# Optimization experiments

Measured on AMD Instinct MI355X. Metric: run time of the kernel, lower is better.

The kernel has to match this reference:

```python
import jax, jax.numpy as jnp
import numpy as np

D_MODEL = 1024
N_HEAD = 16
D_HEAD = D_MODEL // N_HEAD
N_EXPERTS = 8
TOP_K = 2
D_FF = 4096
EPS = 1e-6


def setup_inputs() -> dict:
    key = jax.random.key(0)
    ks = jax.random.split(key, 16)
    s = 0.02  # init scale
    d, dff, E = D_MODEL, D_FF, N_EXPERTS
    return {
        "dec": jax.random.normal(ks[0], (4, 1024, d), jnp.float32),
        "text_encoder": jax.random.normal(ks[1], (4, 512, d), jnp.float32),
        # self-attention projections
        "Wq1": jax.random.normal(ks[2], (d, d), jnp.float32) * s,
        "Wk1": jax.random.normal(ks[3], (d, d), jnp.float32) * s,
        "Wv1": jax.random.normal(ks[4], (d, d), jnp.float32) * s,
        "Wo1": jax.random.normal(ks[5], (d, d), jnp.float32) * s,
        # cross-attention projections
        "Wq2": jax.random.normal(ks[6], (d, d), jnp.float32) * s,
        "Wk2": jax.random.normal(ks[7], (d, d), jnp.float32) * s,
        "Wv2": jax.random.normal(ks[8], (d, d), jnp.float32) * s,
        "Wo2": jax.random.normal(ks[9], (d, d), jnp.float32) * s,
        # shared RMSNorm gain (module uses one norm instance three times)
        "g": jnp.ones((d,), jnp.float32),
        # MoE router + per-expert FFN weights
        "Wg": jax.random.normal(ks[10], (d, E), jnp.float32) * s,
        "W1": jax.random.normal(ks[11], (E, d, dff), jnp.float32) * s,
        "W2": jax.random.normal(ks[12], (E, dff, d), jnp.float32) * s,
    }


def rmsnorm(x, g):
    return x * jax.lax.rsqrt(jnp.mean(x * x, axis=-1, keepdims=True) + EPS) * g


def mha(q_in, k_in, v_in, Wq, Wk, Wv, Wo):
    B, Sq, _ = q_in.shape
    Sk = k_in.shape[1]
    q = (q_in @ Wq).reshape(B, Sq, N_HEAD, D_HEAD)
    k = (k_in @ Wk).reshape(B, Sk, N_HEAD, D_HEAD)
    v = (v_in @ Wv).reshape(B, Sk, N_HEAD, D_HEAD)
    scores = jnp.einsum("bqhd,bkhd->bhqk", q, k) / jnp.sqrt(jnp.asarray(D_HEAD, q.dtype))
    attn = jax.nn.softmax(scores, axis=-1)
    out = jnp.einsum("bhqk,bkhd->bqhd", attn, v).reshape(B, Sq, D_MODEL)
    return out @ Wo


def moe(x, Wg, W1, W2):
    # top-k softmax router, renormalized weights; dense per-expert FFN with combine
    probs = jax.nn.softmax(x @ Wg, axis=-1)              # [B,S,E]
    weights, indices = jax.lax.top_k(probs, TOP_K)        # [B,S,k]
    weights = weights / jnp.sum(weights, axis=-1, keepdims=True)
    # combine[t,e] = sum_k weights[t,k] * (indices[t,k]==e)
    combine = jnp.sum(
        jax.nn.one_hot(indices, N_EXPERTS, dtype=x.dtype) * weights[..., None], axis=-2
    )  # [B,S,E]
    out = jnp.zeros_like(x)
    for e in range(N_EXPERTS):  # fixed small expert loop
        h = jax.nn.relu(x @ W1[e]) @ W2[e]
        out = out + combine[..., e:e + 1] * h
    return weights, indices, out


def reference(dec, text_encoder, Wq1, Wk1, Wv1, Wo1, Wq2, Wk2, Wv2, Wo2, g, Wg, W1, W2):
    # self-attention + residual + RMSNorm (dropout p=0 -> identity)
    x = rmsnorm(mha(dec, dec, dec, Wq1, Wk1, Wv1, Wo1) + dec, g)
    # cross-attention + residual + RMSNorm
    x = rmsnorm(mha(x, text_encoder, text_encoder, Wq2, Wk2, Wv2, Wo2) + x, g)
    # MoE FFN + residual + RMSNorm
    weights, indices, y = moe(x, Wg, W1, W2)
    x = rmsnorm(y + x, g)
    return weights, indices, x
```

## Files before the change

kernel.cpp:

```cpp
#include <hip/hip_runtime.h>
#include <stdint.h>

#define D_    1024
#define BB    4
#define SDEC  1024
#define STXT  512
#define TDEC  4096
#define TTXT  2048
#define NH    16
#define DHD   64
#define NE    8
#define DFF   4096
#define NSLOT 8192
#define MAXYT 24

using u16 = unsigned short;
typedef __attribute__((ext_vector_type(8))) short bf16x8;
typedef __attribute__((ext_vector_type(4))) float f32x4;

__device__ __forceinline__ float bf2f(u16 h) {
    union { unsigned int u; float f; } x; x.u = ((unsigned int)h) << 16; return x.f;
}
__device__ __forceinline__ u16 f2bf(float f) {
    union { float f; unsigned int u; } x; x.f = f;
    unsigned int lsb = (x.u >> 16) & 1u;
    return (u16)((x.u + 0x7fffu + lsb) >> 16);
}

__device__ __forceinline__ void gld16(const u16* g, u16* l) {
    __builtin_amdgcn_global_load_lds((const __attribute__((address_space(1))) void*)g,
                                     (__attribute__((address_space(3))) void*)l,
                                     16, 0, 0);
}

constexpr int BM = 128, BK = 32;

template<int SPLIT, int EPI, int BROWS>
__global__ __launch_bounds__(256) void gemm_bt(
    const u16* __restrict__ AH, const u16* __restrict__ AL,
    const u16* __restrict__ BH, const u16* __restrict__ BL,
    float* __restrict__ Cf, u16* __restrict__ CH, u16* __restrict__ CL,
    int M, int N, int K, int lda, int ldb, int ldc,
    long strA, long strB, long strC)
{
    constexpr int WM = (BROWS == 64) ? 2 : 4;
    constexpr int ASZ = BM * BK, BSZ = BROWS * BK;
    __shared__ u16 smem[(SPLIT ? 2 : 1) * (ASZ + BSZ)];
    u16* sAH = smem;
    u16* sBH = smem + ASZ;
    u16* sAL = SPLIT ? smem + ASZ + BSZ : nullptr;
    u16* sBL = SPLIT ? smem + 2 * ASZ + BSZ : nullptr;

    const int z = blockIdx.z;
    const long zA = (long)z * strA, zB = (long)z * strB, zC = (long)z * strC;

    const int tileM = blockIdx.y * BM, tileN = blockIdx.x * BROWS;
    const int t = threadIdx.x;
    const int sr = t >> 2;
    const int sc = (t & 3) << 3;
    const u16* pA = AH + zA + (long)(tileM + sr) * lda + sc;
    const u16* pB = BH + zB + (long)(tileN + sr) * ldb + sc;
    const u16* pAl = nullptr; const u16* pBl = nullptr;
    if constexpr (SPLIT) {
        pAl = AL + zA + (long)(tileM + sr) * lda + sc;
        pBl = BL + zB + (long)(tileN + sr) * ldb + sc;
    }
    const long hA = 64L * lda, hB = 64L * ldb;

    const int lane = t & 63;
    const int wv = t >> 6;
    const int wr = (BROWS == 64) ? (wv << 5) : ((wv >> 1) << 6);
    const int wc = (BROWS == 64) ? 0 : ((wv & 1) << 6);
    const int fr = lane & 15, kg = lane >> 4;

    f32x4 acc[WM][4];
    const f32x4 vzero = {0.f, 0.f, 0.f, 0.f};
#pragma unroll
    for (int m = 0; m < WM; ++m)
#pragma unroll
        for (int n = 0; n < 4; ++n) acc[m][n] = vzero;

    for (int k0 = 0; k0 < K; k0 += BK) {
        gld16(pA + k0,      sAH + t * 8);
        gld16(pA + k0 + hA, sAH + 2048 + t * 8);
        gld16(pB + k0,      sBH + t * 8);
        if constexpr (BROWS == 128) gld16(pB + k0 + hB, sBH + 2048 + t * 8);
        if constexpr (SPLIT) {
            gld16(pAl + k0,      sAL + t * 8);
            gld16(pAl + k0 + hA, sAL + 2048 + t * 8);
            gld16(pBl + k0,      sBL + t * 8);
            if constexpr (BROWS == 128) gld16(pBl + k0 + hB, sBL + 2048 + t * 8);
        }
        __syncthreads();

        bf16x8 fa[WM], fb[4], fal[WM], fbl[4];
#pragma unroll
        for (int m = 0; m < WM; ++m) {
            fa[m] = *(const bf16x8*)&sAH[(wr + m * 16 + fr) * BK + (kg << 3)];
            if constexpr (SPLIT) fal[m] = *(const bf16x8*)&sAL[(wr + m * 16 + fr) * BK + (kg << 3)];
        }
#pragma unroll
        for (int n = 0; n < 4; ++n) {
            fb[n] = *(const bf16x8*)&sBH[(wc + n * 16 + fr) * BK + (kg << 3)];
            if constexpr (SPLIT) fbl[n] = *(const bf16x8*)&sBL[(wc + n * 16 + fr) * BK + (kg << 3)];
        }
#pragma unroll
        for (int m = 0; m < WM; ++m)
#pragma unroll
            for (int n = 0; n < 4; ++n) {
                acc[m][n] = __builtin_amdgcn_mfma_f32_16x16x32_bf16(fa[m], fb[n], acc[m][n], 0, 0, 0);
                if constexpr (SPLIT) {
                    acc[m][n] = __builtin_amdgcn_mfma_f32_16x16x32_bf16(fa[m],  fbl[n], acc[m][n], 0, 0, 0);
                    acc[m][n] = __builtin_amdgcn_mfma_f32_16x16x32_bf16(fal[m], fb[n],  acc[m][n], 0, 0, 0);
                }
            }
        __syncthreads();
    }

#pragma unroll
    for (int m = 0; m < WM; ++m) {
        const int r0 = tileM + wr + m * 16 + (kg << 2);
#pragma unroll
        for (int n = 0; n < 4; ++n) {
            const int col = tileN + wc + n * 16 + fr;
            if (col >= N) continue;
#pragma unroll
            for (int i = 0; i < 4; ++i) {
                const int r = r0 + i;
                if (r >= M) continue;
                const float v = acc[m][n][i];
                const long off = zC + (long)r * ldc + col;
                if constexpr (EPI == 0) {
                    Cf[off] = v;
                } else if constexpr (EPI == 1) {
                    const u16 h = f2bf(v);
                    CH[off] = h;
                    CL[off] = f2bf(v - bf2f(h));
                } else {
                    CH[off] = f2bf(fmaxf(v, 0.f));
                }
            }
        }
    }
}

template<int EPI>
__global__ __launch_bounds__(256) void gemm_moe(
    const u16* __restrict__ Ag, const u16* __restrict__ BTbase,
    float* __restrict__ Cf, u16* __restrict__ CH,
    int N, int K, int ldc, const int* __restrict__ seg, long btStride, int ntx)
{
    const int bid = blockIdx.x;
    const int e = bid & 7;
    const int rem = bid >> 3;
    const int yt = rem % MAXYT;
    const int xt = rem / MAXYT;
    (void)ntx;

    const int s0 = seg[e], s1 = seg[e + 1];
    const int rowbase = s0 + yt * BM;
    if (rowbase >= s1) return;
    const u16* BT = BTbase + (long)e * btStride;

    __shared__ u16 smem[2 * BM * BK];
    u16* sA = smem;
    u16* sB = smem + BM * BK;

    const int tileN = xt * 128;
    const int t = threadIdx.x;
    const int sr = t >> 2, sc = (t & 3) << 3;
    const u16* pA = Ag + (long)(rowbase + sr) * K + sc;
    const u16* pB = BT + (long)(tileN + sr) * K + sc;
    const long hA = 64L * K, hB = 64L * K;

    const int lane = t & 63;
    const int wv = t >> 6;
    const int wr = (wv >> 1) << 6, wc = (wv & 1) << 6;
    const int fr = lane & 15, kg = lane >> 4;

    f32x4 acc[4][4];
    const f32x4 vzero = {0.f, 0.f, 0.f, 0.f};
#pragma unroll
    for (int m = 0; m < 4; ++m)
#pragma unroll
        for (int n = 0; n < 4; ++n) acc[m][n] = vzero;

    for (int k0 = 0; k0 < K; k0 += BK) {
        gld16(pA + k0,      sA + t * 8);
        gld16(pA + k0 + hA, sA + 2048 + t * 8);
        gld16(pB + k0,      sB + t * 8);
        gld16(pB + k0 + hB, sB + 2048 + t * 8);
        __syncthreads();
        bf16x8 fa[4], fb[4];
#pragma unroll
        for (int m = 0; m < 4; ++m) {
            fa[m] = *(const bf16x8*)&sA[(wr + m * 16 + fr) * BK + (kg << 3)];
            fb[m] = *(const bf16x8*)&sB[(wc + m * 16 + fr) * BK + (kg << 3)];
        }
#pragma unroll
        for (int m = 0; m < 4; ++m)
#pragma unroll
            for (int n = 0; n < 4; ++n)
                acc[m][n] = __builtin_amdgcn_mfma_f32_16x16x32_bf16(fa[m], fb[n], acc[m][n], 0, 0, 0);
        __syncthreads();
    }

#pragma unroll
    for (int m = 0; m < 4; ++m) {
        const int r0 = rowbase + wr + m * 16 + (kg << 2);
#pragma unroll
        for (int n = 0; n < 4; ++n) {
            const int col = tileN + wc + n * 16 + fr;
            if (col >= N) continue;
#pragma unroll
            for (int i = 0; i < 4; ++i) {
                const int r = r0 + i;
                if (r >= s1) continue;
                const float v = acc[m][n][i];
                const long off = (long)r * ldc + col;
                if constexpr (EPI == 0) Cf[off] = v;
                else                    CH[off] = f2bf(fmaxf(v, 0.f));
            }
        }
    }
}

__global__ __launch_bounds__(256) void split2k(const float* __restrict__ in,
                                               u16* __restrict__ oh, u16* __restrict__ ol, long n)
{
    long i = ((long)blockIdx.x * 256 + threadIdx.x) * 4;
    if (i >= n) return;
    float4 v = *(const float4*)(in + i);
    u16 h0 = f2bf(v.x), h1 = f2bf(v.y), h2 = f2bf(v.z), h3 = f2bf(v.w);
    uint2 oo;
    oo.x = (unsigned)h0 | ((unsigned)h1 << 16);
    oo.y = (unsigned)h2 | ((unsigned)h3 << 16);
    *(uint2*)(oh + i) = oo;
    if (ol) {
        u16 l0 = f2bf(v.x - bf2f(h0)), l1 = f2bf(v.y - bf2f(h1));
        u16 l2 = f2bf(v.z - bf2f(h2)), l3 = f2bf(v.w - bf2f(h3));
        uint2 ll;
        ll.x = (unsigned)l0 | ((unsigned)l1 << 16);
        ll.y = (unsigned)l2 | ((unsigned)l3 << 16);
        *(uint2*)(ol + i) = ll;
    }
}

__global__ __launch_bounds__(256) void transpose_split(
    const float* __restrict__ in, u16* __restrict__ oh, u16* __restrict__ ol,
    int R, int C, int ild, long ibs1, long ibs2, int nb2, int old_, long obs)
{
    __shared__ float tile[32][33];
    const int z = blockIdx.z;
    const float* ip = in + (long)(z / nb2) * ibs1 + (long)(z % nb2) * ibs2;
    u16* ohp = oh + (long)z * obs;
    u16* olp = ol ? ol + (long)z * obs : nullptr;
    const int c0 = blockIdx.x * 32, r0 = blockIdx.y * 32;
    const int tx = threadIdx.x & 31, ty = threadIdx.x >> 5;
    for (int i = ty; i < 32; i += 8) {
        int r = r0 + i, c = c0 + tx;
        tile[i][tx] = (r < R && c < C) ? ip[(long)r * ild + c] : 0.f;
    }
    __syncthreads();
    for (int i = ty; i < 32; i += 8) {
        int oc = c0 + i, orr = r0 + tx;
        if (oc < C && orr < R) {
            float v = tile[tx][i];
            u16 h = f2bf(v);
            ohp[(long)oc * old_ + orr] = h;
            if (olp) olp[(long)oc * old_ + orr] = f2bf(v - bf2f(h));
        }
    }
}

__global__ __launch_bounds__(256) void transpose_split_hl(
    const u16* __restrict__ inH, const u16* __restrict__ inL,
    u16* __restrict__ oh, u16* __restrict__ ol,
    int R, int C, int ild, long ibs1, long ibs2, int nb2, int old_, long obs)
{
    __shared__ float tile[32][33];
    const int z = blockIdx.z;
    const long base = (long)(z / nb2) * ibs1 + (long)(z % nb2) * ibs2;
    u16* ohp = oh + (long)z * obs;
    u16* olp = ol + (long)z * obs;
    const int c0 = blockIdx.x * 32, r0 = blockIdx.y * 32;
    const int tx = threadIdx.x & 31, ty = threadIdx.x >> 5;
    for (int i = ty; i < 32; i += 8) {
        int r = r0 + i, c = c0 + tx;
        float v = 0.f;
        if (r < R && c < C) {
            const long o = base + (long)r * ild + c;
            v = bf2f(inH[o]) + bf2f(inL[o]);
        }
        tile[i][tx] = v;
    }
    __syncthreads();
    for (int i = ty; i < 32; i += 8) {
        int oc = c0 + i, orr = r0 + tx;
        if (oc < C && orr < R) {
            float v = tile[tx][i];
            u16 h = f2bf(v);
            ohp[(long)oc * old_ + orr] = h;
            olp[(long)oc * old_ + orr] = f2bf(v - bf2f(h));
        }
    }
}

__global__ __launch_bounds__(256) void softmax_split(
    const float* __restrict__ s, u16* __restrict__ ph, u16* __restrict__ pl,
    int cols, float scale)
{
    const float* p = s + (long)blockIdx.x * cols;
    u16* php = ph + (long)blockIdx.x * cols;
    u16* plp = pl + (long)blockIdx.x * cols;
    const int t = threadIdx.x;
    float v[4];
    int vpt;
    if (cols == 1024) {
        vpt = 4;
        float4 x = ((const float4*)p)[t];
        v[0] = x.x * scale; v[1] = x.y * scale; v[2] = x.z * scale; v[3] = x.w * scale;
    } else {
        vpt = 2;
        float2 x = ((const float2*)p)[t];
        v[0] = x.x * scale; v[1] = x.y * scale; v[2] = -3.4e38f; v[3] = -3.4e38f;
    }
    float mx = fmaxf(fmaxf(v[0], v[1]), fmaxf(v[2], v[3]));
#pragma unroll
    for (int o = 32; o; o >>= 1) mx = fmaxf(mx, __shfl_xor(mx, o));
    __shared__ float sm[4];
    const int wv = t >> 6, ln = t & 63;
    if (ln == 0) sm[wv] = mx;
    __syncthreads();
    mx = fmaxf(fmaxf(sm[0], sm[1]), fmaxf(sm[2], sm[3]));
    float sum = 0.f;
    for (int i = 0; i < vpt; ++i) { v[i] = expf(v[i] - mx); sum += v[i]; }
#pragma unroll
    for (int o = 32; o; o >>= 1) sum += __shfl_xor(sum, o);
    __shared__ float ss[4];
    if (ln == 0) ss[wv] = sum;
    __syncthreads();
    sum = ss[0] + ss[1] + ss[2] + ss[3];
    const float inv = 1.f / sum;
    if (cols == 1024) {
        float q0 = v[0] * inv, q1 = v[1] * inv, q2 = v[2] * inv, q3 = v[3] * inv;
        u16 h0 = f2bf(q0), h1 = f2bf(q1), h2 = f2bf(q2), h3 = f2bf(q3);
        uint2 hh; hh.x = (unsigned)h0 | ((unsigned)h1 << 16); hh.y = (unsigned)h2 | ((unsigned)h3 << 16);
        ((uint2*)php)[t] = hh;
        u16 l0 = f2bf(q0 - bf2f(h0)), l1 = f2bf(q1 - bf2f(h1));
        u16 l2 = f2bf(q2 - bf2f(h2)), l3 = f2bf(q3 - bf2f(h3));
        uint2 ll; ll.x = (unsigned)l0 | ((unsigned)l1 << 16); ll.y = (unsigned)l2 | ((unsigned)l3 << 16);
        ((uint2*)plp)[t] = ll;
    } else {
        float q0 = v[0] * inv, q1 = v[1] * inv;
        u16 h0 = f2bf(q0), h1 = f2bf(q1);
        ((unsigned*)php)[t] = (unsigned)h0 | ((unsigned)h1 << 16);
        u16 l0 = f2bf(q0 - bf2f(h0)), l1 = f2bf(q1 - bf2f(h1));
        ((unsigned*)plp)[t] = (unsigned)l0 | ((unsigned)l1 << 16);
    }
}

__global__ __launch_bounds__(256) void add_rmsnorm(
    const float* __restrict__ a, const float* __restrict__ b, const float* __restrict__ g,
    float* __restrict__ xo, u16* __restrict__ xh, u16* __restrict__ xl)
{
    const long row = blockIdx.x;
    const int t = threadIdx.x;
    const float* pa = a + row * D_;
    const float* pb = b + row * D_;
    float v[4]; double ssq = 0.0;
#pragma unroll
    for (int i = 0; i < 4; ++i) {
        int c = t + (i << 8);
        v[i] = pa[c] + pb[c];
        ssq += (double)v[i] * v[i];
    }
#pragma unroll
    for (int o = 32; o; o >>= 1) ssq += __shfl_xor(ssq, o);
    __shared__ double sd[4];
    if ((t & 63) == 0) sd[t >> 6] = ssq;
    __syncthreads();
    ssq = sd[0] + sd[1] + sd[2] + sd[3];
    const float rs = (float)(1.0 / sqrt(ssq * (1.0 / 1024.0) + 1e-6));
#pragma unroll
    for (int i = 0; i < 4; ++i) {
        int c = t + (i << 8);
        float o = v[i] * rs * g[c];
        xo[row * D_ + c] = o;
        if (xh) {
            u16 h = f2bf(o);
            xh[row * D_ + c] = h;
            if (xl) xl[row * D_ + c] = f2bf(o - bf2f(h));
        }
    }
}

__global__ __launch_bounds__(256) void router_topk(
    const float* __restrict__ x2, const float* __restrict__ Wg,
    float* __restrict__ outw, float* __restrict__ outi,
    int* __restrict__ idx, float* __restrict__ tokw, int* __restrict__ counts, int T)
{
    const int wid = (int)((blockIdx.x * 256 + threadIdx.x) >> 6);
    const int lane = threadIdx.x & 63;
    if (wid >= T) return;
    float acc[NE];
#pragma unroll
    for (int e = 0; e < NE; ++e) acc[e] = 0.f;
    const float* xr = x2 + (long)wid * D_;
    for (int i = 0; i < 16; ++i) {
        float xv = xr[i * 64 + lane];
        const float* wr = Wg + (long)(i * 64 + lane) * NE;
#pragma unroll
        for (int e = 0; e < NE; ++e) acc[e] += xv * wr[e];
    }
#pragma unroll
    for (int e = 0; e < NE; ++e)
#pragma unroll
        for (int o = 32; o; o >>= 1) acc[e] += __shfl_xor(acc[e], o);
    if (lane == 0) {
        float m = acc[0];
#pragma unroll
        for (int e = 1; e < NE; ++e) m = fmaxf(m, acc[e]);
        float p[NE], s = 0.f;
#pragma unroll
        for (int e = 0; e < NE; ++e) { p[e] = expf(acc[e] - m); s += p[e]; }
        const float invs = 1.f / s;
#pragma unroll
        for (int e = 0; e < NE; ++e) p[e] *= invs;
        int e0 = 0;
#pragma unroll
        for (int e = 1; e < NE; ++e) if (p[e] > p[e0]) e0 = e;
        int e1 = (e0 == 0) ? 1 : 0;
#pragma unroll
        for (int e = 0; e < NE; ++e) if (e != e0 && e != e1 && p[e] > p[e1]) e1 = e;
        float w0 = p[e0], w1 = p[e1];
        const float sw = 1.f / (w0 + w1);
        w0 *= sw; w1 *= sw;
        outw[2 * wid] = w0;      outw[2 * wid + 1] = w1;
        outi[2 * wid] = (float)e0; outi[2 * wid + 1] = (float)e1;
        idx[2 * wid] = e0;       idx[2 * wid + 1] = e1;
        tokw[2 * wid] = w0;      tokw[2 * wid + 1] = w1;
        atomicAdd(&counts[e0], 1);
        atomicAdd(&counts[e1], 1);
    }
}

__global__ void scan8(const int* __restrict__ counts, int* __restrict__ seg, int* __restrict__ cursor)
{
    if (threadIdx.x == 0 && blockIdx.x == 0) {
        int a = 0;
        for (int e = 0; e < NE; ++e) { seg[e] = a; cursor[e] = a; a += counts[e]; }
        seg[NE] = a;
    }
}

__global__ __launch_bounds__(256) void scatter_slots(
    const int* __restrict__ idx, int* __restrict__ cursor,
    int* __restrict__ row_token, int* __restrict__ slot_of, int T)
{
    const int t = blockIdx.x * 256 + threadIdx.x;
    if (t >= T) return;
#pragma unroll
    for (int k = 0; k < 2; ++k) {
        const int e = idx[2 * t + k];
        const int pos = atomicAdd(&cursor[e], 1);
        row_token[pos] = t;
        slot_of[2 * t + k] = pos;
    }
}

__global__ __launch_bounds__(256) void gather_bf16(
    const float* __restrict__ x2, const int* __restrict__ row_token, u16* __restrict__ Xg)
{
    const int r = blockIdx.x;
    const int t = threadIdx.x;
    const float* src = x2 + (long)row_token[r] * D_ + t * 4;
    float4 v = *(const float4*)src;
    uint2 oo;
    oo.x = (unsigned)f2bf(v.x) | ((unsigned)f2bf(v.y) << 16);
    oo.y = (unsigned)f2bf(v.z) | ((unsigned)f2bf(v.w) << 16);
    *(uint2*)(Xg + (long)r * D_ + t * 4) = oo;
}

__global__ __launch_bounds__(256) void combine_rmsnorm(
    const float* __restrict__ Y, const int* __restrict__ slot_of, const float* __restrict__ tokw,
    const float* __restrict__ x2, const float* __restrict__ g, float* __restrict__ out)
{
    const long tr = blockIdx.x;
    const int t = threadIdx.x;
    const int s0 = slot_of[2 * tr], s1 = slot_of[2 * tr + 1];
    const float w0 = tokw[2 * tr], w1 = tokw[2 * tr + 1];
    const float* y0 = Y + (long)s0 * D_;
    const float* y1 = Y + (long)s1 * D_;
    const float* xr = x2 + tr * D_;
    float v[4]; double ssq = 0.0;
#pragma unroll
    for (int i = 0; i < 4; ++i) {
        int c = t + (i << 8);
        v[i] = w0 * y0[c] + w1 * y1[c] + xr[c];
        ssq += (double)v[i] * v[i];
    }
#pragma unroll
    for (int o = 32; o; o >>= 1) ssq += __shfl_xor(ssq, o);
    __shared__ double sd[4];
    if ((t & 63) == 0) sd[t >> 6] = ssq;
    __syncthreads();
    ssq = sd[0] + sd[1] + sd[2] + sd[3];
    const float rs = (float)(1.0 / sqrt(ssq * (1.0 / 1024.0) + 1e-6));
#pragma unroll
    for (int i = 0; i < 4; ++i) {
        int c = t + (i << 8);
        out[tr * D_ + c] = v[i] * rs * g[c];
    }
}

__global__ void sentinel(float* o) { o[0] = 12345.0f; }

extern "C" void kernel_launch(void* const* d_in, const int* in_sizes, int n_in,
                              void* d_out, int out_size, void* d_ws, size_t ws_size,
                              hipStream_t stream)
{
    const float* dec = (const float*)d_in[0];
    const float* te  = (const float*)d_in[1];
    const float* Win[8] = { (const float*)d_in[2], (const float*)d_in[3], (const float*)d_in[4],
                            (const float*)d_in[5], (const float*)d_in[6], (const float*)d_in[7],
                            (const float*)d_in[8], (const float*)d_in[9] };
    const float* g  = (const float*)d_in[10];
    const float* Wg = (const float*)d_in[11];
    const float* W1 = (const float*)d_in[12];
    const float* W2 = (const float*)d_in[13];
    float* outw = (float*)d_out;
    float* outi = outw + 2 * TDEC;
    float* outx = outw + 4 * TDEC;

    char* ws = (char*)d_ws;
    size_t off = 0;
    auto A = [&](size_t bytes) -> char* {
        char* p = ws + off;
        off += (bytes + 255) & ~(size_t)255;
        return p;
    };

    u16* decH = (u16*)A((size_t)TDEC * D_ * 2);
    u16* decL = (u16*)A((size_t)TDEC * D_ * 2);
    u16* teH  = (u16*)A((size_t)TTXT * D_ * 2);
    u16* teL  = (u16*)A((size_t)TTXT * D_ * 2);
    u16* wtHall = (u16*)A((size_t)8 * D_ * D_ * 2);
    u16* wtLall = (u16*)A((size_t)8 * D_ * D_ * 2);
    float* x1f = (float*)A((size_t)TDEC * D_ * 4);
    float* x2f = (float*)A((size_t)TDEC * D_ * 4);
    float* tokw = (float*)A(NSLOT * 4);
    int* idx    = (int*)A(NSLOT * 4);
    int* counts = (int*)A(256);
    int* seg    = (int*)A(256);
    int* cursor = (int*)A(256);
    int* row_token = (int*)A(NSLOT * 4);
    int* slot_of   = (int*)A(NSLOT * 4);

    const size_t Rbase = off;
    float* scores = (float*)A((size_t)NH * SDEC * SDEC * 4);
    u16* PH = (u16*)A((size_t)NH * SDEC * SDEC * 2);
    u16* PL = (u16*)A((size_t)NH * SDEC * SDEC * 2);
    u16* qkvH = (u16*)A((size_t)TDEC * 3 * D_ * 2);
    u16* qkvL = (u16*)A((size_t)TDEC * 3 * D_ * 2);
    u16* q2H  = (u16*)A((size_t)TDEC * D_ * 2);
    u16* q2L  = (u16*)A((size_t)TDEC * D_ * 2);
    u16* kv2H = (u16*)A((size_t)TTXT * 2 * D_ * 2);
    u16* kv2L = (u16*)A((size_t)TTXT * 2 * D_ * 2);
    u16* vTH = (u16*)A((size_t)TDEC * D_ * 2);
    u16* vTL = (u16*)A((size_t)TDEC * D_ * 2);
    u16* aoH = (u16*)A((size_t)TDEC * D_ * 2);
    u16* aoL = (u16*)A((size_t)TDEC * D_ * 2);
    u16* x1H = (u16*)A((size_t)TDEC * D_ * 2);
    u16* x1L = (u16*)A((size_t)TDEC * D_ * 2);
    float* of = (float*)A((size_t)TDEC * D_ * 4);
    const size_t attnEnd = off;

    off = Rbase;
    u16* W1T  = (u16*)A((size_t)NE * DFF * D_ * 2);
    u16* W2T  = (u16*)A((size_t)NE * D_ * DFF * 2);
    u16* Xg   = (u16*)A((size_t)(NSLOT + 128) * D_ * 2);
    u16* Hb   = (u16*)A((size_t)(NSLOT + 128) * DFF * 2);
    float* Yseg = (float*)A((size_t)NSLOT * D_ * 4);
    const size_t needed = (off > attnEnd ? off : attnEnd);

    if (ws_size < needed) {
        sentinel<<<1, 1, 0, stream>>>(outw);
        return;
    }

    const dim3 blk(256);

    split2k<<<dim3((TDEC * D_) / 1024), blk, 0, stream>>>(dec, decH, decL, (long)TDEC * D_);
    split2k<<<dim3((TTXT * D_) / 1024), blk, 0, stream>>>(te, teH, teL, (long)TTXT * D_);
    for (int i = 0; i < 8; ++i)
        transpose_split<<<dim3(32, 32, 1), blk, 0, stream>>>(Win[i],
            wtHall + (size_t)i * D_ * D_, wtLall + (size_t)i * D_ * D_,
            D_, D_, D_, 0, 0, 1, D_, 0);

    gemm_bt<1, 1, 128><<<dim3(24, 32, 1), blk, 0, stream>>>(decH, decL, wtHall, wtLall,
        nullptr, qkvH, qkvL, TDEC, 3 * D_, D_, D_, D_, 3 * D_, 0, 0, 0);
    transpose_split_hl<<<dim3(2, 32, BB * NH), blk, 0, stream>>>(qkvH + 2 * D_, qkvL + 2 * D_,
        vTH, vTL, SDEC, DHD, 3 * D_, (long)SDEC * 3 * D_, DHD, NH, SDEC, (long)DHD * SDEC);

    for (int b = 0; b < BB; ++b) {
        const long qo3 = (long)b * SDEC * 3 * D_;
        const long qo  = (long)b * SDEC * D_;
        gemm_bt<1, 0, 128><<<dim3(8, 8, NH), blk, 0, stream>>>(
            qkvH + qo3, qkvL + qo3, qkvH + qo3 + D_, qkvL + qo3 + D_,
            scores, nullptr, nullptr, SDEC, SDEC, DHD, 3 * D_, 3 * D_, SDEC,
            DHD, DHD, (long)SDEC * SDEC);
        softmax_split<<<dim3(NH * SDEC), blk, 0, stream>>>(scores, PH, PL, SDEC, 0.125f);
        gemm_bt<1, 1, 64><<<dim3(1, 8, NH), blk, 0, stream>>>(PH, PL,
            vTH + (long)b * NH * DHD * SDEC, vTL + (long)b * NH * DHD * SDEC,
            nullptr, aoH + qo, aoL + qo, SDEC, DHD, SDEC, SDEC, SDEC, D_,
            (long)SDEC * SDEC, (long)DHD * SDEC, DHD);
    }
    gemm_bt<1, 0, 128><<<dim3(8, 32, 1), blk, 0, stream>>>(aoH, aoL,
        wtHall + (size_t)3 * D_ * D_, wtLall + (size_t)3 * D_ * D_,
        of, nullptr, nullptr, TDEC, D_, D_, D_, D_, D_, 0, 0, 0);
    add_rmsnorm<<<dim3(TDEC), blk, 0, stream>>>(of, dec, g, x1f, x1H, x1L);

    gemm_bt<1, 1, 128><<<dim3(8, 32, 1), blk, 0, stream>>>(x1H, x1L,
        wtHall + (size_t)4 * D_ * D_, wtLall + (size_t)4 * D_ * D_,
        nullptr, q2H, q2L, TDEC, D_, D_, D_, D_, D_, 0, 0, 0);
    gemm_bt<1, 1, 128><<<dim3(16, 16, 1), blk, 0, stream>>>(teH, teL,
        wtHall + (size_t)5 * D_ * D_, wtLall + (size_t)5 * D_ * D_,
        nullptr, kv2H, kv2L, TTXT, 2 * D_, D_, D_, D_, 2 * D_, 0, 0, 0);
    transpose_split_hl<<<dim3(2, 16, BB * NH), blk, 0, stream>>>(kv2H + D_, kv2L + D_,
        vTH, vTL, STXT, DHD, 2 * D_, (long)STXT * 2 * D_, DHD, NH, STXT, (long)DHD * STXT);

    for (int b = 0; b < BB; ++b) {
        const long qo  = (long)b * SDEC * D_;
        const long ko2 = (long)b * STXT * 2 * D_;
        gemm_bt<1, 0, 128><<<dim3(4, 8, NH), blk, 0, stream>>>(
            q2H + qo, q2L + qo, kv2H + ko2, kv2L + ko2,
            scores, nullptr, nullptr, SDEC, STXT, DHD, D_, 2 * D_, STXT,
            DHD, DHD, (long)SDEC * STXT);
        softmax_split<<<dim3(NH * SDEC), blk, 0, stream>>>(scores, PH, PL, STXT, 0.125f);
        gemm_bt<1, 1, 64><<<dim3(1, 8, NH), blk, 0, stream>>>(PH, PL,
            vTH + (long)b * NH * DHD * STXT, vTL + (long)b * NH * DHD * STXT,
            nullptr, aoH + qo, aoL + qo, SDEC, DHD, STXT, STXT, STXT, D_,
            (long)SDEC * STXT, (long)DHD * STXT, DHD);
    }
    gemm_bt<1, 0, 128><<<dim3(8, 32, 1), blk, 0, stream>>>(aoH, aoL,
        wtHall + (size_t)7 * D_ * D_, wtLall + (size_t)7 * D_ * D_,
        of, nullptr, nullptr, TDEC, D_, D_, D_, D_, D_, 0, 0, 0);
    add_rmsnorm<<<dim3(TDEC), blk, 0, stream>>>(of, x1f, g, x2f, nullptr, nullptr);

    hipMemsetAsync(counts, 0, 32, stream);
    router_topk<<<dim3(TDEC / 4), blk, 0, stream>>>(x2f, Wg, outw, outi, idx, tokw, counts, TDEC);
    scan8<<<1, 64, 0, stream>>>(counts, seg, cursor);
    scatter_slots<<<dim3(TDEC / 256), blk, 0, stream>>>(idx, cursor, row_token, slot_of, TDEC);
    gather_bf16<<<dim3(NSLOT), blk, 0, stream>>>(x2f, row_token, Xg);

    transpose_split<<<dim3(DFF / 32, D_ / 32, NE), blk, 0, stream>>>(W1, W1T, nullptr,
        D_, DFF, DFF, (long)D_ * DFF, 0, 1, D_, (long)DFF * D_);
    transpose_split<<<dim3(D_ / 32, DFF / 32, NE), blk, 0, stream>>>(W2, W2T, nullptr,
        DFF, D_, D_, (long)D_ * DFF, 0, 1, DFF, (long)D_ * DFF);
    gemm_moe<2><<<dim3(8 * MAXYT * (DFF / 128)), blk, 0, stream>>>(Xg, W1T,
        nullptr, Hb, DFF, D_, DFF, seg, (long)DFF * D_, DFF / 128);
    gemm_moe<0><<<dim3(8 * MAXYT * (D_ / 128)), blk, 0, stream>>>(Hb, W2T,
        Yseg, nullptr, D_, DFF, D_, seg, (long)D_ * DFF, D_ / 128);
    combine_rmsnorm<<<dim3(TDEC), blk, 0, stream>>>(Yseg, slot_of, tokw, x2f, g, outx);

    (void)in_sizes; (void)n_in; (void)out_size;
}
```

Measured before the change: 1.488 ms.

## Rewrite MoE grouped GEMM with 256x256 tiles and multi-stage LDS pipeline

Replaces the 128x128 single-buffered MoE expert GEMM with a 512-thread kernel that computes 256x256 tiles. It uses a 4-deep ring of global-to-LDS stages with an XOR swizzle, double-buffered register fragments, explicit waitcnt plus barrier, and raised priority for the MFMA blocks. The larger tile is meant to increase operand reuse, and the pipeline is meant to hide global load latency behind matrix math. In exchange, the 128 KB of LDS and the large accumulator set limit occupancy and may cause register spills. The larger tile also wastes more work on partial tiles at expert segment boundaries, and the gather buffers are padded to match.

```diff
diff --git a/kernel.cpp b/kernel.cpp
--- a/kernel.cpp
+++ b/kernel.cpp
@@ -12,7 +12,7 @@
 #define NE    8
 #define DFF   4096
 #define NSLOT 8192
-#define MAXYT 24
+#define MAXYT2 16
 
 using u16 = unsigned short;
 typedef __attribute__((ext_vector_type(8))) short bf16x8;
@@ -145,73 +145,109 @@
 }
 
 template<int EPI>
-__global__ __launch_bounds__(256) void gemm_moe(
+__global__ __launch_bounds__(512, 2) void gemm256_moe(
     const u16* __restrict__ Ag, const u16* __restrict__ BTbase,
     float* __restrict__ Cf, u16* __restrict__ CH,
-    int N, int K, int ldc, const int* __restrict__ seg, long btStride, int ntx)
-{
+    int N, int K, int ldc, const int* __restrict__ seg, long btStride)
+{
+    __shared__ u16 smem[65536];
+
     const int bid = blockIdx.x;
     const int e = bid & 7;
     const int rem = bid >> 3;
-    const int yt = rem % MAXYT;
-    const int xt = rem / MAXYT;
-    (void)ntx;
+    const int yt = rem % MAXYT2;
+    const int xt = rem / MAXYT2;
 
     const int s0 = seg[e], s1 = seg[e + 1];
-    const int rowbase = s0 + yt * BM;
+    const int rowbase = s0 + yt * 256;
     if (rowbase >= s1) return;
     const u16* BT = BTbase + (long)e * btStride;
-
-    __shared__ u16 smem[2 * BM * BK];
-    u16* sA = smem;
-    u16* sB = smem + BM * BK;
-
-    const int tileN = xt * 128;
+    const int tileN = xt * 256;
+
     const int t = threadIdx.x;
-    const int sr = t >> 2, sc = (t & 3) << 3;
-    const u16* pA = Ag + (long)(rowbase + sr) * K + sc;
-    const u16* pB = BT + (long)(tileN + sr) * K + sc;
-    const long hA = 64L * K, hB = 64L * K;
-
     const int lane = t & 63;
     const int wv = t >> 6;
-    const int wr = (wv >> 1) << 6, wc = (wv & 1) << 6;
+    const int wmr = wv >> 2;
+    const int wnc = wv & 3;
     const int fr = lane & 15, kg = lane >> 4;
-
-    f32x4 acc[4][4];
+    const int kk8 = ((kg ^ (fr & 3)) << 3);
+
+    const int q0 = t ^ ((t >> 2) & 3);
+    const int q1 = (t + 512) ^ (((t + 512) >> 2) & 3);
+    const long ofsA0 = (long)(q0 >> 2) * K + (q0 & 3) * 8;
+    const long ofsA1 = (long)(q1 >> 2) * K + (q1 & 3) * 8;
+    const long ofsB0 = ofsA0, ofsB1 = ofsA1;
+    const u16* pAs = Ag + (long)rowbase * K;
+    const u16* pBs = BT + (long)tileN * K;
+
+#define STAGE4(ks) { const int s_ = (ks) & 3; const long k0_ = (long)(ks) * 32; \
+    gld16(pAs + k0_ + ofsA0, smem + s_ * 8192 + t * 8); \
+    gld16(pAs + k0_ + ofsA1, smem + s_ * 8192 + 4096 + t * 8); \
+    gld16(pBs + k0_ + ofsB0, smem + 32768 + s_ * 8192 + t * 8); \
+    gld16(pBs + k0_ + ofsB1, smem + 32768 + s_ * 8192 + 4096 + t * 8); }
+
+#define READF(AA, BB, ks) { const int s_ = (ks) & 3; \
+    const u16* sa_ = smem + s_ * 8192; \
+    const u16* sb_ = smem + 32768 + s_ * 8192; \
+    _Pragma("unroll") \
+    for (int m_ = 0; m_ < 8; ++m_) \
+        AA[m_] = *(const bf16x8*)&sa_[(wmr * 128 + m_ * 16 + fr) * 32 + kk8]; \
+    _Pragma("unroll") \
+    for (int n_ = 0; n_ < 4; ++n_) \
+        BB[n_] = *(const bf16x8*)&sb_[(wnc * 64 + n_ * 16 + fr) * 32 + kk8]; }
+
+#define MFMAS(AA, BB) { __builtin_amdgcn_s_setprio(1); \
+    _Pragma("unroll") \
+    for (int m_ = 0; m_ < 8; ++m_) \
+    _Pragma("unroll") \
+    for (int n_ = 0; n_ < 4; ++n_) \
+        acc[m_][n_] = __builtin_amdgcn_mfma_f32_16x16x32_bf16(AA[m_], BB[n_], acc[m_][n_], 0, 0, 0); \
+    __builtin_amdgcn_s_setprio(0); }
+
+#define ENDBAR(tt_) { asm volatile("s_waitcnt lgkmcnt(0)" ::: "memory"); \
+    if ((tt_) >= NT - 3) { asm volatile("s_waitcnt vmcnt(0)" ::: "memory"); } \
+    else                 { asm volatile("s_waitcnt vmcnt(4)" ::: "memory"); } \
+    __builtin_amdgcn_s_barrier(); }
+
+    f32x4 acc[8][4];
     const f32x4 vzero = {0.f, 0.f, 0.f, 0.f};
 #pragma unroll
-    for (int m = 0; m < 4; ++m)
+    for (int m = 0; m < 8; ++m)
 #pragma unroll
         for (int n = 0; n < 4; ++n) acc[m][n] = vzero;
 
-    for (int k0 = 0; k0 < K; k0 += BK) {
-        gld16(pA + k0,      sA + t * 8);
-        gld16(pA + k0 + hA, sA + 2048 + t * 8);
-        gld16(pB + k0,      sB + t * 8);
-        gld16(pB + k0 + hB, sB + 2048 + t * 8);
-        __syncthreads();
-        bf16x8 fa[4], fb[4];
-#pragma unroll
-        for (int m = 0; m < 4; ++m) {
-            fa[m] = *(const bf16x8*)&sA[(wr + m * 16 + fr) * BK + (kg << 3)];
-            fb[m] = *(const bf16x8*)&sB[(wc + m * 16 + fr) * BK + (kg << 3)];
-        }
-#pragma unroll
-        for (int m = 0; m < 4; ++m)
-#pragma unroll
-            for (int n = 0; n < 4; ++n)
-                acc[m][n] = __builtin_amdgcn_mfma_f32_16x16x32_bf16(fa[m], fb[n], acc[m][n], 0, 0, 0);
-        __syncthreads();
-    }
-
-#pragma unroll
-    for (int m = 0; m < 4; ++m) {
-        const int r0 = rowbase + wr + m * 16 + (kg << 2);
+    const int NT = K >> 5;
+
+    STAGE4(0); STAGE4(1); STAGE4(2);
+    asm volatile("s_waitcnt vmcnt(4)" ::: "memory");
+    __builtin_amdgcn_s_barrier();
+
+    bf16x8 a0[8], b0[4], a1[8], b1[4];
+    READF(a0, b0, 0);
+
+    for (int tt = 0; tt < NT; tt += 2) {
+        if (tt + 3 < NT) STAGE4(tt + 3);
+        if (tt + 1 < NT) READF(a1, b1, tt + 1);
+        MFMAS(a0, b0);
+        ENDBAR(tt);
+        const int tu = tt + 1;
+        if (tu + 3 < NT) STAGE4(tu + 3);
+        if (tu + 1 < NT) READF(a0, b0, tu + 1);
+        MFMAS(a1, b1);
+        ENDBAR(tu);
+    }
+
+#undef STAGE4
+#undef READF
+#undef MFMAS
+#undef ENDBAR
+
+#pragma unroll
+    for (int m = 0; m < 8; ++m) {
+        const int r0 = rowbase + wmr * 128 + m * 16 + (kg << 2);
 #pragma unroll
         for (int n = 0; n < 4; ++n) {
-            const int col = tileN + wc + n * 16 + fr;
-            if (col >= N) continue;
+            const int col = tileN + wnc * 64 + n * 16 + fr;
 #pragma unroll
             for (int i = 0; i < 4; ++i) {
                 const int r = r0 + i;
@@ -579,8 +615,8 @@
     off = Rbase;
     u16* W1T  = (u16*)A((size_t)NE * DFF * D_ * 2);
     u16* W2T  = (u16*)A((size_t)NE * D_ * DFF * 2);
-    u16* Xg   = (u16*)A((size_t)(NSLOT + 128) * D_ * 2);
-    u16* Hb   = (u16*)A((size_t)(NSLOT + 128) * DFF * 2);
+    u16* Xg   = (u16*)A((size_t)(NSLOT + 256) * D_ * 2);
+    u16* Hb   = (u16*)A((size_t)(NSLOT + 256) * DFF * 2);
     float* Yseg = (float*)A((size_t)NSLOT * D_ * 4);
     const size_t needed = (off > attnEnd ? off : attnEnd);
 
@@ -658,10 +694,10 @@
         D_, DFF, DFF, (long)D_ * DFF, 0, 1, D_, (long)DFF * D_);
     transpose_split<<<dim3(D_ / 32, DFF / 32, NE), blk, 0, stream>>>(W2, W2T, nullptr,
         DFF, D_, D_, (long)D_ * DFF, 0, 1, DFF, (long)D_ * DFF);
-    gemm_moe<2><<<dim3(8 * MAXYT * (DFF / 128)), blk, 0, stream>>>(Xg, W1T,
-        nullptr, Hb, DFF, D_, DFF, seg, (long)DFF * D_, DFF / 128);
-    gemm_moe<0><<<dim3(8 * MAXYT * (D_ / 128)), blk, 0, stream>>>(Hb, W2T,
-        Yseg, nullptr, D_, DFF, D_, seg, (long)D_ * DFF, D_ / 128);
+    gemm256_moe<2><<<dim3(8 * MAXYT2 * (DFF / 256)), dim3(512), 0, stream>>>(Xg, W1T,
+        nullptr, Hb, DFF, D_, DFF, seg, (long)DFF * D_);
+    gemm256_moe<0><<<dim3(8 * MAXYT2 * (D_ / 256)), dim3(512), 0, stream>>>(Hb, W2T,
+        Yseg, nullptr, D_, DFF, D_, seg, (long)D_ * DFF);
     combine_rmsnorm<<<dim3(TDEC), blk, 0, stream>>>(Yseg, slot_of, tokw, x2f, g, outx);
 
     (void)in_sizes; (void)n_in; (void)out_size;
```

After: 1.472 ms. About the same (-1.1%).

## Rewrite MoE GEMMs as persistent descriptor-driven kernel with double buffering and split-K

Applied to the files above, without the earlier changes.

Replaces the per-expert gemm_moe grid, which launched many early-exiting blocks, with a persistent 1024-block kernel that walks a compact tile descriptor list built by scan_desc. It adds double-buffered LDS staging with an XOR swizzle to reduce bank conflicts, and splits the second FFN GEMM's K dimension in two. The two partial outputs are summed in combine_rmsnorm, and the second partial buffer reuses the W1T workspace. The aim is to remove wasted blocks and load imbalance and to overlap global loads with MFMA work. The cost is extra descriptor memsets, partial-sum traffic and more LDS per block.

```diff
diff --git a/kernel.cpp b/kernel.cpp
--- a/kernel.cpp
+++ b/kernel.cpp
@@ -12,7 +12,9 @@
 #define NE    8
 #define DFF   4096
 #define NSLOT 8192
-#define MAXYT 24
+#define ND1   8192
+#define ND2   4096
+#define MOEGRID 1024
 
 using u16 = unsigned short;
 typedef __attribute__((ext_vector_type(8))) short bf16x8;
@@ -145,81 +147,94 @@
 }
 
 template<int EPI>
-__global__ __launch_bounds__(256) void gemm_moe(
-    const u16* __restrict__ Ag, const u16* __restrict__ BTbase,
-    float* __restrict__ Cf, u16* __restrict__ CH,
-    int N, int K, int ldc, const int* __restrict__ seg, long btStride, int ntx)
-{
-    const int bid = blockIdx.x;
-    const int e = bid & 7;
-    const int rem = bid >> 3;
-    const int yt = rem % MAXYT;
-    const int xt = rem / MAXYT;
-    (void)ntx;
-
-    const int s0 = seg[e], s1 = seg[e + 1];
-    const int rowbase = s0 + yt * BM;
-    if (rowbase >= s1) return;
-    const u16* BT = BTbase + (long)e * btStride;
-
-    __shared__ u16 smem[2 * BM * BK];
-    u16* sA = smem;
-    u16* sB = smem + BM * BK;
-
-    const int tileN = xt * 128;
+__global__ __launch_bounds__(256, 4) void moe_gemm2(
+    const u16* __restrict__ Ag, int lda,
+    const u16* __restrict__ BTbase, int ldb, long btStride,
+    float* __restrict__ Cf0, float* __restrict__ Cf1, u16* __restrict__ CH, int ldc,
+    const int4* __restrict__ desc, int ndesc, int Kiter)
+{
+    __shared__ u16 smem[16384];
     const int t = threadIdx.x;
-    const int sr = t >> 2, sc = (t & 3) << 3;
-    const u16* pA = Ag + (long)(rowbase + sr) * K + sc;
-    const u16* pB = BT + (long)(tileN + sr) * K + sc;
-    const long hA = 64L * K, hB = 64L * K;
-
-    const int lane = t & 63;
-    const int wv = t >> 6;
+    const int lane = t & 63, wv = t >> 6;
     const int wr = (wv >> 1) << 6, wc = (wv & 1) << 6;
     const int fr = lane & 15, kg = lane >> 4;
-
-    f32x4 acc[4][4];
-    const f32x4 vzero = {0.f, 0.f, 0.f, 0.f};
-#pragma unroll
-    for (int m = 0; m < 4; ++m)
-#pragma unroll
-        for (int n = 0; n < 4; ++n) acc[m][n] = vzero;
-
-    for (int k0 = 0; k0 < K; k0 += BK) {
-        gld16(pA + k0,      sA + t * 8);
-        gld16(pA + k0 + hA, sA + 2048 + t * 8);
-        gld16(pB + k0,      sB + t * 8);
-        gld16(pB + k0 + hB, sB + 2048 + t * 8);
-        __syncthreads();
-        bf16x8 fa[4], fb[4];
+    const int nks = Kiter >> 5;
+
+    const int rS = t >> 2;
+    const int cS = ((t & 3) ^ ((t >> 3) & 3)) << 3;
+
+    int ldsA[4], ldsB[4];
+#pragma unroll
+    for (int m = 0; m < 4; ++m) {
+        const int ra = wr + m * 16 + fr;
+        ldsA[m] = ra * 32 + ((kg ^ ((ra >> 1) & 3)) << 3);
+        const int rb = wc + m * 16 + fr;
+        ldsB[m] = rb * 32 + ((kg ^ ((rb >> 1) & 3)) << 3);
+    }
+
+    for (int p = blockIdx.x; p < ndesc; p += MOEGRID) {
+        const int4 d = desc[p];
+        if (d.x < 0) continue;
+        const int rowbase = d.x, colbase = d.y & 0xFFFF, e = d.y >> 16;
+        const int kbase = d.z, s1 = d.w;
+        const u16* paS = Ag + (long)(rowbase + rS) * lda + kbase + cS;
+        const u16* pbS = BTbase + (long)e * btStride + (long)(colbase + rS) * ldb + kbase + cS;
+        const long hA = 64L * lda, hB = 64L * ldb;
+
+        f32x4 acc[4][4];
+        const f32x4 vzero = {0.f, 0.f, 0.f, 0.f};
+#pragma unroll
+        for (int m = 0; m < 4; ++m)
+#pragma unroll
+            for (int n = 0; n < 4; ++n) acc[m][n] = vzero;
+
+#define STG(ks, buf) { const long k0_ = (long)(ks) << 5; \
+        u16* sA_ = smem + (buf) * 8192; \
+        gld16(paS + k0_,      sA_ + t * 8); \
+        gld16(paS + k0_ + hA, sA_ + 2048 + t * 8); \
+        gld16(pbS + k0_,      sA_ + 4096 + t * 8); \
+        gld16(pbS + k0_ + hB, sA_ + 6144 + t * 8); }
+
+        STG(0, 0);
+        asm volatile("s_waitcnt vmcnt(0)" ::: "memory");
+        __builtin_amdgcn_s_barrier();
+
+        for (int ks = 0; ks < nks; ++ks) {
+            const int cur = ks & 1;
+            if (ks + 1 < nks) STG(ks + 1, cur ^ 1);
+            const u16* sA = smem + cur * 8192;
+            const u16* sB = sA + 4096;
+            bf16x8 fa[4], fb[4];
+#pragma unroll
+            for (int m = 0; m < 4; ++m) fa[m] = *(const bf16x8*)&sA[ldsA[m]];
+#pragma unroll
+            for (int n = 0; n < 4; ++n) fb[n] = *(const bf16x8*)&sB[ldsB[n]];
+#pragma unroll
+            for (int m = 0; m < 4; ++m)
+#pragma unroll
+                for (int n = 0; n < 4; ++n)
+                    acc[m][n] = __builtin_amdgcn_mfma_f32_16x16x32_bf16(fa[m], fb[n], acc[m][n], 0, 0, 0);
+            asm volatile("s_waitcnt vmcnt(0)" ::: "memory");
+            __builtin_amdgcn_s_barrier();
+        }
+#undef STG
+
+        float* __restrict__ C = (EPI == 0) ? ((kbase == 0) ? Cf0 : Cf1) : nullptr;
 #pragma unroll
         for (int m = 0; m < 4; ++m) {
-            fa[m] = *(const bf16x8*)&sA[(wr + m * 16 + fr) * BK + (kg << 3)];
-            fb[m] = *(const bf16x8*)&sB[(wc + m * 16 + fr) * BK + (kg << 3)];
-        }
-#pragma unroll
-        for (int m = 0; m < 4; ++m)
-#pragma unroll
-            for (int n = 0; n < 4; ++n)
-                acc[m][n] = __builtin_amdgcn_mfma_f32_16x16x32_bf16(fa[m], fb[n], acc[m][n], 0, 0, 0);
-        __syncthreads();
-    }
-
-#pragma unroll
-    for (int m = 0; m < 4; ++m) {
-        const int r0 = rowbase + wr + m * 16 + (kg << 2);
-#pragma unroll
-        for (int n = 0; n < 4; ++n) {
-            const int col = tileN + wc + n * 16 + fr;
-            if (col >= N) continue;
-#pragma unroll
-            for (int i = 0; i < 4; ++i) {
-                const int r = r0 + i;
-                if (r >= s1) continue;
-                const float v = acc[m][n][i];
-                const long off = (long)r * ldc + col;
-                if constexpr (EPI == 0) Cf[off] = v;
-                else                    CH[off] = f2bf(fmaxf(v, 0.f));
+            const int r0 = rowbase + wr + m * 16 + (kg << 2);
+#pragma unroll
+            for (int n = 0; n < 4; ++n) {
+                const int col = colbase + wc + n * 16 + fr;
+#pragma unroll
+                for (int i = 0; i < 4; ++i) {
+                    const int r = r0 + i;
+                    if (r >= s1) continue;
+                    const float v = acc[m][n][i];
+                    const long off = (long)r * ldc + col;
+                    if constexpr (EPI == 0) C[off] = v;
+                    else                    CH[off] = f2bf(fmaxf(v, 0.f));
+                }
             }
         }
     }
@@ -445,12 +460,29 @@
     }
 }
 
-__global__ void scan8(const int* __restrict__ counts, int* __restrict__ seg, int* __restrict__ cursor)
-{
-    if (threadIdx.x == 0 && blockIdx.x == 0) {
+__global__ void scan_desc(const int* __restrict__ counts, int* __restrict__ cursor,
+                          int4* __restrict__ d1, int4* __restrict__ d2)
+{
+    __shared__ int sseg[NE + 1];
+    if (threadIdx.x == 0) {
         int a = 0;
-        for (int e = 0; e < NE; ++e) { seg[e] = a; cursor[e] = a; a += counts[e]; }
-        seg[NE] = a;
+        for (int e = 0; e < NE; ++e) { sseg[e] = a; cursor[e] = a; a += counts[e]; }
+        sseg[NE] = a;
+    }
+    __syncthreads();
+    const int e = threadIdx.x;
+    if (e < NE) {
+        const int s0 = sseg[e], s1 = sseg[e + 1];
+        const int nyt = (s1 - s0 + 127) >> 7;
+        for (int xt = 0; xt < 32; ++xt)
+            for (int yt = 0; yt < nyt; ++yt)
+                d1[e + 8 * (xt * nyt + yt)] =
+                    make_int4(s0 + yt * 128, (xt * 128) | (e << 16), 0, s1);
+        for (int kh = 0; kh < 2; ++kh)
+            for (int xt = 0; xt < 8; ++xt)
+                for (int yt = 0; yt < nyt; ++yt)
+                    d2[e + 8 * ((kh * 8 + xt) * nyt + yt)] =
+                        make_int4(s0 + yt * 128, (xt * 128) | (e << 16), kh * 2048, s1);
     }
 }
 
@@ -483,21 +515,24 @@
 }
 
 __global__ __launch_bounds__(256) void combine_rmsnorm(
-    const float* __restrict__ Y, const int* __restrict__ slot_of, const float* __restrict__ tokw,
+    const float* __restrict__ Y0, const float* __restrict__ Y1,
+    const int* __restrict__ slot_of, const float* __restrict__ tokw,
     const float* __restrict__ x2, const float* __restrict__ g, float* __restrict__ out)
 {
     const long tr = blockIdx.x;
     const int t = threadIdx.x;
     const int s0 = slot_of[2 * tr], s1 = slot_of[2 * tr + 1];
     const float w0 = tokw[2 * tr], w1 = tokw[2 * tr + 1];
-    const float* y0 = Y + (long)s0 * D_;
-    const float* y1 = Y + (long)s1 * D_;
+    const float* ya0 = Y0 + (long)s0 * D_;
+    const float* yb0 = Y1 + (long)s0 * D_;
+    const float* ya1 = Y0 + (long)s1 * D_;
+    const float* yb1 = Y1 + (long)s1 * D_;
     const float* xr = x2 + tr * D_;
     float v[4]; double ssq = 0.0;
 #pragma unroll
     for (int i = 0; i < 4; ++i) {
         int c = t + (i << 8);
-        v[i] = w0 * y0[c] + w1 * y1[c] + xr[c];
+        v[i] = w0 * (ya0[c] + yb0[c]) + w1 * (ya1[c] + yb1[c]) + xr[c];
         ssq += (double)v[i] * v[i];
     }
 #pragma unroll
@@ -552,10 +587,11 @@
     float* tokw = (float*)A(NSLOT * 4);
     int* idx    = (int*)A(NSLOT * 4);
     int* counts = (int*)A(256);
-    int* seg    = (int*)A(256);
     int* cursor = (int*)A(256);
     int* row_token = (int*)A(NSLOT * 4);
     int* slot_of   = (int*)A(NSLOT * 4);
+    int4* desc1 = (int4*)A((size_t)ND1 * 16);
+    int4* desc2 = (int4*)A((size_t)ND2 * 16);
 
     const size_t Rbase = off;
     float* scores = (float*)A((size_t)NH * SDEC * SDEC * 4);
@@ -579,9 +615,10 @@
     off = Rbase;
     u16* W1T  = (u16*)A((size_t)NE * DFF * D_ * 2);
     u16* W2T  = (u16*)A((size_t)NE * D_ * DFF * 2);
-    u16* Xg   = (u16*)A((size_t)(NSLOT + 128) * D_ * 2);
-    u16* Hb   = (u16*)A((size_t)(NSLOT + 128) * DFF * 2);
+    u16* Xg   = (u16*)A((size_t)(NSLOT + 256) * D_ * 2);
+    u16* Hb   = (u16*)A((size_t)(NSLOT + 256) * DFF * 2);
     float* Yseg = (float*)A((size_t)NSLOT * D_ * 4);
+    float* Ypart1 = (float*)W1T;
     const size_t needed = (off > attnEnd ? off : attnEnd);
 
     if (ws_size < needed) {
@@ -649,8 +686,10 @@
     add_rmsnorm<<<dim3(TDEC), blk, 0, stream>>>(of, x1f, g, x2f, nullptr, nullptr);
 
     hipMemsetAsync(counts, 0, 32, stream);
+    hipMemsetAsync(desc1, 0xFF, (size_t)ND1 * 16, stream);
+    hipMemsetAsync(desc2, 0xFF, (size_t)ND2 * 16, stream);
     router_topk<<<dim3(TDEC / 4), blk, 0, stream>>>(x2f, Wg, outw, outi, idx, tokw, counts, TDEC);
-    scan8<<<1, 64, 0, stream>>>(counts, seg, cursor);
+    scan_desc<<<1, 64, 0, stream>>>(counts, cursor, desc1, desc2);
     scatter_slots<<<dim3(TDEC / 256), blk, 0, stream>>>(idx, cursor, row_token, slot_of, TDEC);
     gather_bf16<<<dim3(NSLOT), blk, 0, stream>>>(x2f, row_token, Xg);
 
@@ -658,11 +697,11 @@
         D_, DFF, DFF, (long)D_ * DFF, 0, 1, D_, (long)DFF * D_);
     transpose_split<<<dim3(D_ / 32, DFF / 32, NE), blk, 0, stream>>>(W2, W2T, nullptr,
         DFF, D_, D_, (long)D_ * DFF, 0, 1, DFF, (long)D_ * DFF);
-    gemm_moe<2><<<dim3(8 * MAXYT * (DFF / 128)), blk, 0, stream>>>(Xg, W1T,
-        nullptr, Hb, DFF, D_, DFF, seg, (long)DFF * D_, DFF / 128);
-    gemm_moe<0><<<dim3(8 * MAXYT * (D_ / 128)), blk, 0, stream>>>(Hb, W2T,
-        Yseg, nullptr, D_, DFF, D_, seg, (long)D_ * DFF, D_ / 128);
-    combine_rmsnorm<<<dim3(TDEC), blk, 0, stream>>>(Yseg, slot_of, tokw, x2f, g, outx);
+    moe_gemm2<2><<<dim3(MOEGRID), blk, 0, stream>>>(Xg, D_, W1T, D_, (long)DFF * D_,
+        nullptr, nullptr, Hb, DFF, desc1, ND1, 1024);
+    moe_gemm2<0><<<dim3(MOEGRID), blk, 0, stream>>>(Hb, DFF, W2T, DFF, (long)D_ * DFF,
+        Yseg, Ypart1, nullptr, D_, desc2, ND2, 2048);
+    combine_rmsnorm<<<dim3(TDEC), blk, 0, stream>>>(Yseg, Ypart1, slot_of, tokw, x2f, g, outx);
 
     (void)in_sizes; (void)n_in; (void)out_size;
 }
```

Result: faster. 1.453 ms (-2.4%).
